# Performance work log

Hardware: AMD Instinct MI355X
Metric: run time of the kernel (lower is better)

The kernel has to match this reference:

```python
import jax, jax.numpy as jnp
import numpy as np

# Faithful JAX port of Attention_concat (concat-style PAM).
# The original intent: energy[b,i,j] = concat_conv([q[b,:,i]; k[b,:,j]]) which is
# algebraically separable: energy = (q^T wq)[:, :, None] + (k^T wk)[:, None, :].
# attention = energy / (H*W) (no softmax), out = value @ attention, out = gamma*out + x.

B, C, H, W = 4, 256, 64, 64
K_RED = 4
INTER = C // K_RED  # 64


def setup_inputs() -> dict:
    key = jax.random.key(0)
    ks = jax.random.split(key, 9)
    s = 0.02
    x = jax.random.normal(ks[0], (B, C, H, W), dtype=jnp.float32)
    Wq = jax.random.normal(ks[1], (INTER, C), dtype=jnp.float32) * s
    bq = jax.random.normal(ks[2], (INTER,), dtype=jnp.float32) * s
    Wk = jax.random.normal(ks[3], (INTER, C), dtype=jnp.float32) * s
    bk = jax.random.normal(ks[4], (INTER,), dtype=jnp.float32) * s
    Wc = jax.random.normal(ks[5], (2 * INTER,), dtype=jnp.float32) * s  # concat_conv weight, no bias
    Wv = jax.random.normal(ks[6], (C, C), dtype=jnp.float32) * s
    bv = jax.random.normal(ks[7], (C,), dtype=jnp.float32) * s
    gamma = jax.random.normal(ks[8], (1,), dtype=jnp.float32) * 0.1  # nonzero so output depends on attention
    return {"x": x, "Wq": Wq, "bq": bq, "Wk": Wk, "bk": bk, "Wc": Wc, "Wv": Wv, "bv": bv, "gamma": gamma}


def reference(x, Wq, bq, Wk, bk, Wc, Wv, bv, gamma):
    b, c, h, w = x.shape
    n = h * w
    inter = Wq.shape[0]
    xf = x.reshape(b, c, n)  # [B, C, N]
    # 1x1 convs == per-position channel matmuls
    q = jnp.einsum("bcn,oc->bon", xf, Wq) + bq[None, :, None]  # [B, inter, N]
    k = jnp.einsum("bcn,oc->bon", xf, Wk) + bk[None, :, None]  # [B, inter, N]
    wq, wk = Wc[:inter], Wc[inter:]
    # separable concat-conv score: energy[b,i,j] = <q[b,:,i], wq> + <k[b,:,j], wk>
    eq = jnp.einsum("bcn,c->bn", q, wq)  # [B, N]
    ek = jnp.einsum("bcn,c->bn", k, wk)  # [B, N]
    attention = (eq[:, :, None] + ek[:, None, :]) / jnp.asarray(n, x.dtype)  # [B, N, N]
    v = jnp.einsum("bcn,oc->bon", xf, Wv) + bv[None, :, None]  # [B, C, N]
    out = jnp.einsum("bcn,bnm->bcm", v, attention).reshape(b, c, h, w)
    return gamma * out + x
```

## Files before the change

### kernel.cpp

```cpp
#include <hip/hip_runtime.h>

#define B_DIM 4
#define C_DIM 256
#define N_DIM 4096
#define INTER 64

#define EQ_OFF   0
#define EK_OFF   (B_DIM*N_DIM)
#define SX_OFF   (2*B_DIM*N_DIM)
#define SXE_OFF  (SX_OFF + B_DIM*C_DIM)
#define UQ_OFF   (SXE_OFF + B_DIM*C_DIM)
#define UK_OFF   (UQ_OFF + C_DIM)
#define CQ_OFF   (UK_OFF + C_DIM)
#define CK_OFF   (CQ_OFF + 1)
#define SEQ_OFF  (CK_OFF + 1)
#define SV_OFF   (SEQ_OFF + B_DIM)
#define SVE_OFF  (SV_OFF + B_DIM*C_DIM)

__device__ inline float wave_red_sum(float v) {
    #pragma unroll
    for (int off = 32; off > 0; off >>= 1) v += __shfl_down(v, off, 64);
    return v;
}

__global__ void k_prep(const float* __restrict__ Wq, const float* __restrict__ bq,
                       const float* __restrict__ Wk, const float* __restrict__ bk,
                       const float* __restrict__ Wc, float* __restrict__ ws) {
    int c = threadIdx.x;
    float uq = 0.f, uk = 0.f;
    #pragma unroll 8
    for (int o = 0; o < INTER; ++o) {
        uq = fmaf(Wc[o],         Wq[o * C_DIM + c], uq);
        uk = fmaf(Wc[INTER + o], Wk[o * C_DIM + c], uk);
    }
    ws[UQ_OFF + c] = uq;
    ws[UK_OFF + c] = uk;
    if (c == 0) { float s = 0.f; for (int o = 0; o < INTER; ++o) s = fmaf(Wc[o], bq[o], s); ws[CQ_OFF] = s; }
    if (c == 1) { float s = 0.f; for (int o = 0; o < INTER; ++o) s = fmaf(Wc[INTER + o], bk[o], s); ws[CK_OFF] = s; }
}

__global__ void k_eqek(const float* __restrict__ x, const float* __restrict__ ws_ro,
                       float* __restrict__ ws) {
    const int lane  = threadIdx.x & 63;
    const int wid   = threadIdx.x >> 6;
    const int n     = blockIdx.x * 64 + lane;
    const int b     = blockIdx.y;
    const int cbase = wid * 64;
    const float* xp = x + ((size_t)b * C_DIM + cbase) * N_DIM + n;
    const float* uq = ws_ro + UQ_OFF + cbase;
    const float* uk = ws_ro + UK_OFF + cbase;
    float aq = 0.f, ak = 0.f;
    #pragma unroll 16
    for (int c = 0; c < 64; ++c) {
        float xv = xp[(size_t)c * N_DIM];
        aq = fmaf(uq[c], xv, aq);
        ak = fmaf(uk[c], xv, ak);
    }
    __shared__ float sq[4][64], sk[4][64];
    sq[wid][lane] = aq;
    sk[wid][lane] = ak;
    __syncthreads();
    if (wid == 0) {
        float tq = sq[0][lane] + sq[1][lane] + sq[2][lane] + sq[3][lane] + ws_ro[CQ_OFF];
        float tk = sk[0][lane] + sk[1][lane] + sk[2][lane] + sk[3][lane] + ws_ro[CK_OFF];
        ws[EQ_OFF + b * N_DIM + n] = tq;
        ws[EK_OFF + b * N_DIM + n] = tk;
    }
}

__global__ void k_rowsums(const float* __restrict__ x, const float* __restrict__ ws_ro,
                          float* __restrict__ ws) {
    const int bc = blockIdx.x;
    const int b  = bc >> 8;
    const int c  = bc & (C_DIM - 1);
    const float4* xp = (const float4*)(x + (size_t)bc * N_DIM);
    const float4* eq = (const float4*)(ws_ro + EQ_OFF + (size_t)b * N_DIM);
    float sx = 0.f, sxe = 0.f, se = 0.f;
    #pragma unroll
    for (int i = threadIdx.x; i < N_DIM / 4; i += 256) {
        float4 xv = xp[i];
        float4 e  = eq[i];
        sx += xv.x + xv.y + xv.z + xv.w;
        sxe = fmaf(xv.x, e.x, sxe); sxe = fmaf(xv.y, e.y, sxe);
        sxe = fmaf(xv.z, e.z, sxe); sxe = fmaf(xv.w, e.w, sxe);
        se += e.x + e.y + e.z + e.w;
    }
    sx  = wave_red_sum(sx);
    sxe = wave_red_sum(sxe);
    se  = wave_red_sum(se);
    __shared__ float red[3][4];
    const int wid = threadIdx.x >> 6, lane = threadIdx.x & 63;
    if (lane == 0) { red[0][wid] = sx; red[1][wid] = sxe; red[2][wid] = se; }
    __syncthreads();
    if (threadIdx.x == 0) {
        ws[SX_OFF + bc]  = red[0][0] + red[0][1] + red[0][2] + red[0][3];
        ws[SXE_OFF + bc] = red[1][0] + red[1][1] + red[1][2] + red[1][3];
        if (c == 0)
            ws[SEQ_OFF + b] = red[2][0] + red[2][1] + red[2][2] + red[2][3];
    }
}

__global__ void k_sv(const float* __restrict__ Wv, const float* __restrict__ bv,
                     const float* __restrict__ ws_ro, float* __restrict__ ws) {
    const int b = blockIdx.x;
    const int c = threadIdx.x;
    __shared__ float sSx[C_DIM], sSxe[C_DIM];
    sSx[c]  = ws_ro[SX_OFF + b * C_DIM + c];
    sSxe[c] = ws_ro[SXE_OFF + b * C_DIM + c];
    __syncthreads();
    const float* wv = Wv + (size_t)c * C_DIM;
    float sv = 0.f, sve = 0.f;
    #pragma unroll 8
    for (int cc = 0; cc < C_DIM; ++cc) {
        float w = wv[cc];
        sv  = fmaf(w, sSx[cc],  sv);
        sve = fmaf(w, sSxe[cc], sve);
    }
    ws[SV_OFF + b * C_DIM + c]  = sv + (float)N_DIM * bv[c];
    ws[SVE_OFF + b * C_DIM + c] = sve + bv[c] * ws_ro[SEQ_OFF + b];
}

__global__ void k_out(const float* __restrict__ x, const float* __restrict__ ws,
                      const float* __restrict__ gamma, float* __restrict__ out) {
    const float ginv = gamma[0] / (float)N_DIM;
    const size_t total4 = (size_t)B_DIM * C_DIM * N_DIM / 4;
    for (size_t i = (size_t)blockIdx.x * blockDim.x + threadIdx.x; i < total4;
         i += (size_t)gridDim.x * blockDim.x) {
        const size_t e = i * 4;
        const int m  = (int)(e & (N_DIM - 1));
        const int bc = (int)(e >> 12);
        const int b  = bc >> 8;
        const float4 xv  = ((const float4*)x)[i];
        const float4 ekv = *(const float4*)(ws + EK_OFF + (size_t)b * N_DIM + m);
        const float t1 = ws[SV_OFF + bc]  * ginv;
        const float t2 = ws[SVE_OFF + bc] * ginv;
        float4 o;
        o.x = fmaf(ekv.x, t1, t2) + xv.x;
        o.y = fmaf(ekv.y, t1, t2) + xv.y;
        o.z = fmaf(ekv.z, t1, t2) + xv.z;
        o.w = fmaf(ekv.w, t1, t2) + xv.w;
        ((float4*)out)[i] = o;
    }
}

extern "C" void kernel_launch(void* const* d_in, const int* in_sizes, int n_in,
                              void* d_out, int out_size, void* d_ws, size_t ws_size,
                              hipStream_t stream) {
    const float* x     = (const float*)d_in[0];
    const float* Wq    = (const float*)d_in[1];
    const float* bq    = (const float*)d_in[2];
    const float* Wk    = (const float*)d_in[3];
    const float* bk    = (const float*)d_in[4];
    const float* Wc    = (const float*)d_in[5];
    const float* Wv    = (const float*)d_in[6];
    const float* bv    = (const float*)d_in[7];
    const float* gamma = (const float*)d_in[8];
    float* out = (float*)d_out;
    float* ws  = (float*)d_ws;

    k_prep<<<1, 256, 0, stream>>>(Wq, bq, Wk, bk, Wc, ws);

    dim3 g1(N_DIM / 64, B_DIM);
    k_eqek<<<g1, 256, 0, stream>>>(x, ws, ws);

    k_rowsums<<<B_DIM * C_DIM, 256, 0, stream>>>(x, ws, ws);

    k_sv<<<B_DIM, 256, 0, stream>>>(Wv, bv, ws, ws);

    k_out<<<2048, 256, 0, stream>>>(x, ws, gamma, out);
}
```

Baseline: 115.1 us.

## Fuse prep, eq/ek, and row-sum passes into one LDS-tiled kernel over x

Merges the weight-projection prep, the eq/ek projection and the per-channel row sums into a single kernel. Each block stages a 256x64 tile of x in padded LDS, computes eq/ek from it and emits partial sums of x and x*eq per tile. This removes one full read of x and two launches. A small second kernel reduces the partials and computes Wv products with more blocks and vectorized weight loads. Each block now recomputes the tiny uq/uk projection redundantly, the workspace holds partial-sum buffers, and the output kernel launches more blocks.

```diff
diff --git a/kernel.cpp b/kernel.cpp
--- a/kernel.cpp
+++ b/kernel.cpp
@@ -4,18 +4,14 @@
 #define C_DIM 256
 #define N_DIM 4096
 #define INTER 64
+#define LDS_PAD 68
 
-#define EQ_OFF   0
-#define EK_OFF   (B_DIM*N_DIM)
-#define SX_OFF   (2*B_DIM*N_DIM)
-#define SXE_OFF  (SX_OFF + B_DIM*C_DIM)
-#define UQ_OFF   (SXE_OFF + B_DIM*C_DIM)
-#define UK_OFF   (UQ_OFF + C_DIM)
-#define CQ_OFF   (UK_OFF + C_DIM)
-#define CK_OFF   (CQ_OFF + 1)
-#define SEQ_OFF  (CK_OFF + 1)
-#define SV_OFF   (SEQ_OFF + B_DIM)
-#define SVE_OFF  (SV_OFF + B_DIM*C_DIM)
+#define EK_OFF   0
+#define PSEQ_OFF 16384
+#define PSX_OFF  16640
+#define PSXE_OFF 82176
+#define SV_OFF   147712
+#define SVE_OFF  148736
 
 __device__ inline float wave_red_sum(float v) {
     #pragma unroll
@@ -23,105 +19,131 @@
     return v;
 }
 
-__global__ void k_prep(const float* __restrict__ Wq, const float* __restrict__ bq,
-                       const float* __restrict__ Wk, const float* __restrict__ bk,
-                       const float* __restrict__ Wc, float* __restrict__ ws) {
-    int c = threadIdx.x;
-    float uq = 0.f, uk = 0.f;
-    #pragma unroll 8
-    for (int o = 0; o < INTER; ++o) {
-        uq = fmaf(Wc[o],         Wq[o * C_DIM + c], uq);
-        uk = fmaf(Wc[INTER + o], Wk[o * C_DIM + c], uk);
+__global__ __launch_bounds__(256) void k_fuse(
+        const float* __restrict__ x,
+        const float* __restrict__ Wq, const float* __restrict__ bq,
+        const float* __restrict__ Wk, const float* __restrict__ bk,
+        const float* __restrict__ Wc, float* __restrict__ ws) {
+    __shared__ float xt[C_DIM][LDS_PAD];
+    __shared__ float uqs[C_DIM], uks[C_DIM];
+    __shared__ float sq[4][64], sk[4][64];
+    __shared__ float eq_s[64];
+    __shared__ float cqk[2];
+    const int t  = threadIdx.x;
+    const int nb = blockIdx.x;
+    const int b  = blockIdx.y;
+    const int n0 = nb * 64;
+
+    {
+        float uq = 0.f, uk = 0.f;
+        #pragma unroll 8
+        for (int o = 0; o < INTER; ++o) {
+            uq = fmaf(Wc[o],         Wq[o * C_DIM + t], uq);
+            uk = fmaf(Wc[INTER + o], Wk[o * C_DIM + t], uk);
+        }
+        uqs[t] = uq; uks[t] = uk;
+        if (t == 0) { float s = 0.f; for (int o = 0; o < INTER; ++o) s = fmaf(Wc[o], bq[o], s); cqk[0] = s; }
+        if (t == 1) { float s = 0.f; for (int o = 0; o < INTER; ++o) s = fmaf(Wc[INTER + o], bk[o], s); cqk[1] = s; }
     }
-    ws[UQ_OFF + c] = uq;
-    ws[UK_OFF + c] = uk;
-    if (c == 0) { float s = 0.f; for (int o = 0; o < INTER; ++o) s = fmaf(Wc[o], bq[o], s); ws[CQ_OFF] = s; }
-    if (c == 1) { float s = 0.f; for (int o = 0; o < INTER; ++o) s = fmaf(Wc[INTER + o], bk[o], s); ws[CK_OFF] = s; }
-}
 
-__global__ void k_eqek(const float* __restrict__ x, const float* __restrict__ ws_ro,
-                       float* __restrict__ ws) {
-    const int lane  = threadIdx.x & 63;
-    const int wid   = threadIdx.x >> 6;
-    const int n     = blockIdx.x * 64 + lane;
-    const int b     = blockIdx.y;
-    const int cbase = wid * 64;
-    const float* xp = x + ((size_t)b * C_DIM + cbase) * N_DIM + n;
-    const float* uq = ws_ro + UQ_OFF + cbase;
-    const float* uk = ws_ro + UK_OFF + cbase;
-    float aq = 0.f, ak = 0.f;
-    #pragma unroll 16
-    for (int c = 0; c < 64; ++c) {
-        float xv = xp[(size_t)c * N_DIM];
-        aq = fmaf(uq[c], xv, aq);
-        ak = fmaf(uk[c], xv, ak);
+    const float4* x4 = (const float4*)x;
+    #pragma unroll
+    for (int i = 0; i < 16; ++i) {
+        const int f = i * 256 + t;
+        const int c = f >> 4, q = f & 15;
+        float4 v = x4[((size_t)b * C_DIM + c) * (N_DIM / 4) + (n0 >> 2) + q];
+        *(float4*)&xt[c][4 * q] = v;
     }
-    __shared__ float sq[4][64], sk[4][64];
-    sq[wid][lane] = aq;
-    sk[wid][lane] = ak;
     __syncthreads();
-    if (wid == 0) {
-        float tq = sq[0][lane] + sq[1][lane] + sq[2][lane] + sq[3][lane] + ws_ro[CQ_OFF];
-        float tk = sk[0][lane] + sk[1][lane] + sk[2][lane] + sk[3][lane] + ws_ro[CK_OFF];
-        ws[EQ_OFF + b * N_DIM + n] = tq;
-        ws[EK_OFF + b * N_DIM + n] = tk;
+
+    const int w = t >> 6, l = t & 63;
+    {
+        float aq = 0.f, ak = 0.f;
+        const int cb = w * 64;
+        #pragma unroll 16
+        for (int c = 0; c < 64; ++c) {
+            float xv = xt[cb + c][l];
+            aq = fmaf(uqs[cb + c], xv, aq);
+            ak = fmaf(uks[cb + c], xv, ak);
+        }
+        sq[w][l] = aq; sk[w][l] = ak;
+    }
+    __syncthreads();
+    if (w == 0) {
+        float tq = sq[0][l] + sq[1][l] + sq[2][l] + sq[3][l] + cqk[0];
+        float tk = sk[0][l] + sk[1][l] + sk[2][l] + sk[3][l] + cqk[1];
+        ws[EK_OFF + b * N_DIM + n0 + l] = tk;
+        eq_s[l] = tq;
+        float se = wave_red_sum(tq);
+        if (l == 0) ws[PSEQ_OFF + b * 64 + nb] = se;
+    }
+    __syncthreads();
+
+    {
+        float sx = 0.f, sxe = 0.f;
+        const float4* row = (const float4*)&xt[t][0];
+        const float4* ev  = (const float4*)&eq_s[0];
+        #pragma unroll
+        for (int i = 0; i < 16; ++i) {
+            float4 xv = row[i];
+            float4 e  = ev[i];
+            sx += xv.x + xv.y + xv.z + xv.w;
+            sxe = fmaf(xv.x, e.x, sxe); sxe = fmaf(xv.y, e.y, sxe);
+            sxe = fmaf(xv.z, e.z, sxe); sxe = fmaf(xv.w, e.w, sxe);
+        }
+        ws[PSX_OFF  + (size_t)(b * 64 + nb) * C_DIM + t] = sx;
+        ws[PSXE_OFF + (size_t)(b * 64 + nb) * C_DIM + t] = sxe;
     }
 }
 
-__global__ void k_rowsums(const float* __restrict__ x, const float* __restrict__ ws_ro,
-                          float* __restrict__ ws) {
-    const int bc = blockIdx.x;
-    const int b  = bc >> 8;
-    const int c  = bc & (C_DIM - 1);
-    const float4* xp = (const float4*)(x + (size_t)bc * N_DIM);
-    const float4* eq = (const float4*)(ws_ro + EQ_OFF + (size_t)b * N_DIM);
-    float sx = 0.f, sxe = 0.f, se = 0.f;
+__global__ __launch_bounds__(256) void k_sv2(
+        const float* __restrict__ Wv, const float* __restrict__ bv,
+        const float* __restrict__ ws_ro, float* __restrict__ ws) {
+    const int cg = blockIdx.x;
+    const int b  = blockIdx.y;
+    const int t  = threadIdx.x;
+    __shared__ float sSx[C_DIM], sSxe[C_DIM];
+    __shared__ float sSeq;
+    float sx = 0.f, sxe = 0.f;
+    #pragma unroll 8
+    for (int nb = 0; nb < 64; ++nb) {
+        sx  += ws_ro[PSX_OFF  + (size_t)(b * 64 + nb) * C_DIM + t];
+        sxe += ws_ro[PSXE_OFF + (size_t)(b * 64 + nb) * C_DIM + t];
+    }
+    sSx[t] = sx; sSxe[t] = sxe;
+    if (t < 64) {
+        float se = wave_red_sum(ws_ro[PSEQ_OFF + b * 64 + t]);
+        if (t == 0) sSeq = se;
+    }
+    __syncthreads();
+    const int cl = t >> 2, s = t & 3;
+    const int c  = cg * 64 + cl;
+    const float4* wr = (const float4*)(Wv + (size_t)c * C_DIM + 64 * s);
+    float sv = 0.f, sve = 0.f;
     #pragma unroll
-    for (int i = threadIdx.x; i < N_DIM / 4; i += 256) {
-        float4 xv = xp[i];
-        float4 e  = eq[i];
-        sx += xv.x + xv.y + xv.z + xv.w;
-        sxe = fmaf(xv.x, e.x, sxe); sxe = fmaf(xv.y, e.y, sxe);
-        sxe = fmaf(xv.z, e.z, sxe); sxe = fmaf(xv.w, e.w, sxe);
-        se += e.x + e.y + e.z + e.w;
+    for (int i = 0; i < 16; ++i) {
+        float4 wv4 = wr[i];
+        const int base = 64 * s + 4 * i;
+        sv  = fmaf(wv4.x, sSx[base],     sv);
+        sv  = fmaf(wv4.y, sSx[base + 1], sv);
+        sv  = fmaf(wv4.z, sSx[base + 2], sv);
+        sv  = fmaf(wv4.w, sSx[base + 3], sv);
+        sve = fmaf(wv4.x, sSxe[base],     sve);
+        sve = fmaf(wv4.y, sSxe[base + 1], sve);
+        sve = fmaf(wv4.z, sSxe[base + 2], sve);
+        sve = fmaf(wv4.w, sSxe[base + 3], sve);
     }
-    sx  = wave_red_sum(sx);
-    sxe = wave_red_sum(sxe);
-    se  = wave_red_sum(se);
-    __shared__ float red[3][4];
-    const int wid = threadIdx.x >> 6, lane = threadIdx.x & 63;
-    if (lane == 0) { red[0][wid] = sx; red[1][wid] = sxe; red[2][wid] = se; }
-    __syncthreads();
-    if (threadIdx.x == 0) {
-        ws[SX_OFF + bc]  = red[0][0] + red[0][1] + red[0][2] + red[0][3];
-        ws[SXE_OFF + bc] = red[1][0] + red[1][1] + red[1][2] + red[1][3];
-        if (c == 0)
-            ws[SEQ_OFF + b] = red[2][0] + red[2][1] + red[2][2] + red[2][3];
+    sv  += __shfl_down(sv, 2, 64);  sv  += __shfl_down(sv, 1, 64);
+    sve += __shfl_down(sve, 2, 64); sve += __shfl_down(sve, 1, 64);
+    if (s == 0) {
+        ws[SV_OFF  + b * C_DIM + c] = sv + (float)N_DIM * bv[c];
+        ws[SVE_OFF + b * C_DIM + c] = sve + bv[c] * sSeq;
     }
 }
 
-__global__ void k_sv(const float* __restrict__ Wv, const float* __restrict__ bv,
-                     const float* __restrict__ ws_ro, float* __restrict__ ws) {
-    const int b = blockIdx.x;
-    const int c = threadIdx.x;
-    __shared__ float sSx[C_DIM], sSxe[C_DIM];
-    sSx[c]  = ws_ro[SX_OFF + b * C_DIM + c];
-    sSxe[c] = ws_ro[SXE_OFF + b * C_DIM + c];
-    __syncthreads();
-    const float* wv = Wv + (size_t)c * C_DIM;
-    float sv = 0.f, sve = 0.f;
-    #pragma unroll 8
-    for (int cc = 0; cc < C_DIM; ++cc) {
-        float w = wv[cc];
-        sv  = fmaf(w, sSx[cc],  sv);
-        sve = fmaf(w, sSxe[cc], sve);
-    }
-    ws[SV_OFF + b * C_DIM + c]  = sv + (float)N_DIM * bv[c];
-    ws[SVE_OFF + b * C_DIM + c] = sve + bv[c] * ws_ro[SEQ_OFF + b];
-}
-
-__global__ void k_out(const float* __restrict__ x, const float* __restrict__ ws,
-                      const float* __restrict__ gamma, float* __restrict__ out) {
+__global__ __launch_bounds__(256) void k_out(
+        const float* __restrict__ x, const float* __restrict__ ws,
+        const float* __restrict__ gamma, float* __restrict__ out) {
     const float ginv = gamma[0] / (float)N_DIM;
     const size_t total4 = (size_t)B_DIM * C_DIM * N_DIM / 4;
     for (size_t i = (size_t)blockIdx.x * blockDim.x + threadIdx.x; i < total4;
@@ -132,7 +154,7 @@
         const int b  = bc >> 8;
         const float4 xv  = ((const float4*)x)[i];
         const float4 ekv = *(const float4*)(ws + EK_OFF + (size_t)b * N_DIM + m);
-        const float t1 = ws[SV_OFF + bc]  * ginv;
+        const float t1 = ws[SV_OFF  + bc] * ginv;
         const float t2 = ws[SVE_OFF + bc] * ginv;
         float4 o;
         o.x = fmaf(ekv.x, t1, t2) + xv.x;
@@ -158,14 +180,11 @@
     float* out = (float*)d_out;
     float* ws  = (float*)d_ws;
 
-    k_prep<<<1, 256, 0, stream>>>(Wq, bq, Wk, bk, Wc, ws);
+    dim3 gA(N_DIM / 64, B_DIM);
+    k_fuse<<<gA, 256, 0, stream>>>(x, Wq, bq, Wk, bk, Wc, ws);
 
-    dim3 g1(N_DIM / 64, B_DIM);
-    k_eqek<<<g1, 256, 0, stream>>>(x, ws, ws);
+    dim3 gB(4, B_DIM);
+    k_sv2<<<gB, 256, 0, stream>>>(Wv, bv, ws, ws);
 
-    k_rowsums<<<B_DIM * C_DIM, 256, 0, stream>>>(x, ws, ws);
-
-    k_sv<<<B_DIM, 256, 0, stream>>>(Wv, bv, ws, ws);
-
-    k_out<<<2048, 256, 0, stream>>>(x, ws, gamma, out);
+    k_out<<<4096, 256, 0, stream>>>(x, ws, gamma, out);
 }
```

After: 104.8 us. 1.1x faster.
